# Kernel tuning notes

Hardware: AMD Instinct MI355X
Metric: run time of the kernel (lower is better)

## Reference

```python
import jax, jax.numpy as jnp
import numpy as np

N = 50000
E = 800000
IN_DIM = 128
HID = 32
HEADS = 8
OUT_DIM = 64
BN_EPS = 1e-5
NEG_SLOPE = 0.2


def batch_norm(x, gamma, beta, mean, var):
    # eval-mode BatchNorm1d using running statistics
    return (x - mean) * jax.lax.rsqrt(var + BN_EPS) * gamma + beta


def gat_conv(x, src, dst, W, att_src, att_dst, heads, out_ch, n):
    """PyG GATConv (shared src/dst lin), self-loops already included in src/dst.
    x: [n, in]; W: [in, heads*out_ch]; att_*: [heads, out_ch].
    Returns [n, heads, out_ch]."""
    h = (x @ W).reshape(n, heads, out_ch)                       # node features per head
    a_s = jnp.einsum('nho,ho->nh', h, att_src)                  # [n, heads]
    a_d = jnp.einsum('nho,ho->nh', h, att_dst)
    e = jax.nn.leaky_relu(a_s[src] + a_d[dst], NEG_SLOPE)       # [e, heads]
    # segment softmax over incoming edges of each dst node
    mx = jax.ops.segment_max(e, dst, num_segments=n)
    ex = jnp.exp(e - mx[dst])
    denom = jax.ops.segment_sum(ex, dst, num_segments=n)
    alpha = ex / (denom[dst] + 1e-16)                           # [e, heads]
    out = jax.ops.segment_sum(alpha[:, :, None] * h[src], dst, num_segments=n)
    return out                                                  # [n, heads, out_ch]


def setup_inputs() -> dict:
    key = jax.random.key(0)
    ks = jax.random.split(key, 24)
    inp = {}
    inp['x'] = jax.random.normal(ks[0], (N, IN_DIM), dtype=jnp.float32)
    inp['edge_index'] = jax.random.randint(ks[1], (2, E), 0, N, dtype=jnp.int64)
    s = 0.05
    inp['W1'] = jax.random.normal(ks[2], (IN_DIM, HEADS * HID), dtype=jnp.float32) * s
    inp['a_src1'] = jax.random.normal(ks[3], (HEADS, HID), dtype=jnp.float32) * s
    inp['a_dst1'] = jax.random.normal(ks[4], (HEADS, HID), dtype=jnp.float32) * s
    inp['b1'] = jnp.zeros((HEADS * HID,), dtype=jnp.float32)
    inp['W2'] = jax.random.normal(ks[5], (HEADS * HID, OUT_DIM), dtype=jnp.float32) * s
    inp['a_src2'] = jax.random.normal(ks[6], (1, OUT_DIM), dtype=jnp.float32) * s
    inp['a_dst2'] = jax.random.normal(ks[7], (1, OUT_DIM), dtype=jnp.float32) * s
    inp['b2'] = jnp.zeros((OUT_DIM,), dtype=jnp.float32)
    # projection Linear(out_dim -> in_dim)
    inp['Wp'] = jax.random.normal(ks[8], (OUT_DIM, IN_DIM), dtype=jnp.float32) * s
    inp['bp'] = jnp.zeros((IN_DIM,), dtype=jnp.float32)
    # BatchNorm params (eval mode running stats)
    for i, d in [(1, HEADS * HID), (2, OUT_DIM), (3, IN_DIM)]:
        k0, k1, k2, k3 = jax.random.split(ks[8 + i], 4)
        inp[f'g{i}'] = 1.0 + 0.1 * jax.random.normal(k0, (d,), dtype=jnp.float32)
        inp[f'be{i}'] = 0.1 * jax.random.normal(k1, (d,), dtype=jnp.float32)
        inp[f'm{i}'] = 0.1 * jax.random.normal(k2, (d,), dtype=jnp.float32)
        inp[f'v{i}'] = jax.random.uniform(k3, (d,), dtype=jnp.float32, minval=0.5, maxval=1.5)
    return inp


def reference(x, edge_index, W1, a_src1, a_dst1, b1, W2, a_src2, a_dst2, b2,
              Wp, bp, g1, be1, m1, v1, g2, be2, m2, v2, g3, be3, m3, v3):
    n = x.shape[0]
    loops = jnp.arange(n, dtype=edge_index.dtype)
    src = jnp.concatenate([edge_index[0], loops])   # add_self_loops=True (PyG default)
    dst = jnp.concatenate([edge_index[1], loops])

    h = gat_conv(x, src, dst, W1, a_src1, a_dst1, HEADS, HID, n)
    h = h.reshape(n, HEADS * HID) + b1              # concat=True
    h = jax.nn.elu(batch_norm(h, g1, be1, m1, v1))  # dropout is no-op in eval

    h = gat_conv(h, src, dst, W2, a_src2, a_dst2, 1, OUT_DIM, n)
    h = h.reshape(n, OUT_DIM) + b2                  # concat=False, heads=1 -> mean == identity
    h = jax.nn.elu(batch_norm(h, g2, be2, m2, v2))

    h = h @ Wp + bp
    return batch_norm(h, g3, be3, m3, v3)
```

## Files before the change

kernel.cpp:

```cpp
#include <hip/hip_runtime.h>
#include <math.h>

#define NEG_SLOPE 0.2f
#define BN_EPS 1e-5f

typedef __bf16 bf16x8 __attribute__((ext_vector_type(8)));
typedef float  f32x4  __attribute__((ext_vector_type(4)));

__device__ __forceinline__ float elu_f(float x){ return x > 0.f ? x : expm1f(x); }
__device__ __forceinline__ float lrelu_f(float x){ return x > 0.f ? x : NEG_SLOPE * x; }

__device__ __forceinline__ float b2f(ushort u){
    union { uint i; float f; } v; v.i = (uint)u << 16; return v.f;
}
__device__ __forceinline__ ushort f2b(float f){
    union { float f; uint i; } v; v.f = f;
    uint r = v.i + 0x7FFFu + ((v.i >> 16) & 1u);
    return (ushort)(r >> 16);
}

__device__ __forceinline__ bool detect_f64(const void* ei, int E, long long N)
{
    const long long* p = (const long long*)ei;
    int lane = threadIdx.x & 63;
    long long v = p[lane % max(1, min(2 * E, 64))];
    bool bad = (v < 0 || v >= N);
    return __ballot(bad) == 0ull;
}

__device__ __forceinline__ void get_edge(const void* ei, int e, int E, bool f64, int& s, int& d)
{
    if (e < E) {
        if (f64) { const long long* p = (const long long*)ei; s = (int)p[e]; d = (int)p[E + e]; }
        else     { const int*       p = (const int*)ei;       s = p[e];      d = p[E + e]; }
    } else {
        s = d = e - E;
    }
}

__global__ void setup_kernel(const void* ei, int E, int N, int* deg, int cx,
    const float* __restrict__ x, ushort* __restrict__ xb,
    const float* __restrict__ W1, const float* __restrict__ W2, const float* __restrict__ Wp,
    ushort* __restrict__ wt1, ushort* __restrict__ wt2, ushort* __restrict__ wtp,
    const float* b1, const float* b2, const float* bp,
    const float* g1, const float* be1, const float* m1, const float* v1,
    const float* g2, const float* be2, const float* m2, const float* v2,
    const float* g3, const float* be3, const float* m3, const float* v3,
    float* par)
{
    int b = blockIdx.x, t = threadIdx.x;
    if (b == 0) {
        { float s = g1[t] * rsqrtf(v1[t] + BN_EPS); par[t] = s;        par[256 + t] = b1[t] * s + be1[t] - m1[t] * s; }
        if (t < 64)  { float s = g2[t] * rsqrtf(v2[t] + BN_EPS); par[512 + t] = s;  par[576 + t] = b2[t] * s + be2[t] - m2[t] * s; }
        if (t < 128) { float s = g3[t] * rsqrtf(v3[t] + BN_EPS); par[640 + t] = s;  par[768 + t] = bp[t] * s + be3[t] - m3[t] * s; }
    } else if (b <= 224) {
        int idx = (b - 1) * 256 + t;
        if (idx < 32768) {
            int n = idx >> 7, k = idx & 127;
            wt1[idx] = f2b(W1[k * 256 + n]);
        } else if (idx < 49152) {
            int j = idx - 32768;
            int n = j >> 8, k = j & 255;
            wt2[j] = f2b(W2[k * 64 + n]);
        } else if (idx < 57344) {
            int j = idx - 49152;
            int n = j >> 6, k = j & 63;
            wtp[j] = f2b(Wp[k * 128 + n]);
        }
    } else if (b < 225 + cx) {
        long long n128 = (long long)N * 128;
        long long idx = ((long long)(b - 225) * 256 + t) * 8;
        if (idx + 7 < n128) {
            float4 v0 = *reinterpret_cast<const float4*>(&x[idx]);
            float4 v1 = *reinterpret_cast<const float4*>(&x[idx + 4]);
            ushort o[8] = { f2b(v0.x), f2b(v0.y), f2b(v0.z), f2b(v0.w),
                            f2b(v1.x), f2b(v1.y), f2b(v1.z), f2b(v1.w) };
            uint4 pk;
            pk.x = (uint)o[0] | ((uint)o[1] << 16);
            pk.y = (uint)o[2] | ((uint)o[3] << 16);
            pk.z = (uint)o[4] | ((uint)o[5] << 16);
            pk.w = (uint)o[6] | ((uint)o[7] << 16);
            *reinterpret_cast<uint4*>(&xb[idx]) = pk;
        } else {
            for (long long q = idx; q < n128; ++q) xb[q] = f2b(x[q]);
        }
    } else {
        bool f64 = detect_f64(ei, E, (long long)N);
        int i = (b - 225 - cx) * 256 + t;
        int ET = E + N;
        if (i < ET) {
            int s, d;
            get_edge(ei, i, E, f64, s, d);
            atomicAdd(&deg[d], 1);
        }
    }
}

__global__ void scan1_kernel(const int* __restrict__ deg, int N, int* __restrict__ bsum)
{
    int b = blockIdx.x, t = threadIdx.x;
    int base = b * 4096 + t * 16;
    int s = 0;
    #pragma unroll
    for (int k = 0; k < 16; k += 4) {
        int idx = base + k;
        if (idx + 3 < N) {
            int4 v = *reinterpret_cast<const int4*>(&deg[idx]);
            s += v.x + v.y + v.z + v.w;
        } else {
            for (int q = 0; q < 4; ++q) if (idx + q < N) s += deg[idx + q];
        }
    }
    #pragma unroll
    for (int off = 1; off < 64; off <<= 1) s += __shfl_xor(s, off);
    __shared__ int wsum[4];
    if ((t & 63) == 0) wsum[t >> 6] = s;
    __syncthreads();
    if (t == 0) bsum[b] = wsum[0] + wsum[1] + wsum[2] + wsum[3];
}

__global__ void scan2_kernel(const int* __restrict__ bsum, int nb, int* __restrict__ bpre)
{
    if (threadIdx.x == 0) {
        int r = 0;
        for (int i = 0; i < nb; ++i) { bpre[i] = r; r += bsum[i]; }
        bpre[nb] = r;
    }
}

__global__ void scan3_kernel(const int* __restrict__ deg, int N,
                             const int* __restrict__ bpre, int nb,
                             int* __restrict__ rowptr, int* __restrict__ fillptr)
{
    int b = blockIdx.x, t = threadIdx.x;
    int base = b * 4096 + t * 16;
    int loc[16];
    int s = 0;
    #pragma unroll
    for (int k = 0; k < 16; ++k) {
        int idx = base + k;
        int d = (idx < N) ? deg[idx] : 0;
        loc[k] = s; s += d;
    }
    int lane = t & 63;
    int incl = s;
    #pragma unroll
    for (int off = 1; off < 64; off <<= 1) {
        int v = __shfl_up(incl, off);
        if (lane >= off) incl += v;
    }
    __shared__ int wsum[4];
    if (lane == 63) wsum[t >> 6] = incl;
    __syncthreads();
    int woff = 0;
    int w = t >> 6;
    for (int i = 0; i < w; ++i) woff += wsum[i];
    int off0 = bpre[b] + woff + incl - s;
    #pragma unroll
    for (int k = 0; k < 16; ++k) {
        int idx = base + k;
        if (idx < N) { rowptr[idx] = off0 + loc[k]; fillptr[idx] = off0 + loc[k]; }
    }
    if (b == 0 && t == 0) rowptr[N] = bpre[nb];
}

__global__ void fill_kernel(const void* ei, int E, int N, int* fillptr, int* esrc)
{
    bool f64 = detect_f64(ei, E, (long long)N);
    int i = blockIdx.x * blockDim.x + threadIdx.x;
    int ET = E + N;
    if (i >= ET) return;
    int s, d;
    get_edge(ei, i, E, f64, s, d);
    int pos = atomicAdd(&fillptr[d], 1);
    esrc[pos] = s;
}

template<int ATYPE, int OMODE, int ATT>
__global__ __launch_bounds__(256) void mgemm_kernel(const void* __restrict__ Ap,
    const ushort* __restrict__ Bt, void* __restrict__ Cp, int M, int K, int NC,
    const float* __restrict__ S, const float* __restrict__ Cc,
    const float* __restrict__ att_s, const float* __restrict__ att_d,
    float* __restrict__ as_out, float* __restrict__ ad_out)
{
    const int BM = 128, LDA = 72;
    __shared__ __align__(16) ushort As[BM][LDA];
    __shared__ __align__(16) ushort Bs[64][LDA];
    __shared__ float red[128][2];
    int t = threadIdx.x;
    int m0 = blockIdx.x * BM, n0 = blockIdx.y * 64;
    int w = t >> 6, l = t & 63;
    int wm = w >> 1, wn = w & 1;
    int r16 = l & 15, kg = l >> 4;

    f32x4 acc[4][2];
    #pragma unroll
    for (int mi = 0; mi < 4; ++mi)
        #pragma unroll
        for (int ni = 0; ni < 2; ++ni)
            acc[mi][ni] = (f32x4){0.f, 0.f, 0.f, 0.f};

    for (int kb = 0; kb < K; kb += 64) {
        if (ATYPE == 0) {
            const float* A = (const float*)Ap;
            #pragma unroll
            for (int p = 0; p < 8; ++p) {
                int r = (t >> 4) + p * 16, c4 = (t & 15) * 4;
                int gm = m0 + r;
                float4 v = (gm < M) ? *reinterpret_cast<const float4*>(&A[(size_t)gm * K + kb + c4])
                                    : make_float4(0.f, 0.f, 0.f, 0.f);
                ushort4 u; u.x = f2b(v.x); u.y = f2b(v.y); u.z = f2b(v.z); u.w = f2b(v.w);
                *reinterpret_cast<ushort4*>(&As[r][c4]) = u;
            }
        } else {
            const ushort* A = (const ushort*)Ap;
            #pragma unroll
            for (int p = 0; p < 4; ++p) {
                int r = (t >> 3) + p * 32, c8 = (t & 7) * 8;
                int gm = m0 + r;
                uint4 v = (gm < M) ? *reinterpret_cast<const uint4*>(&A[(size_t)gm * K + kb + c8])
                                   : make_uint4(0u, 0u, 0u, 0u);
                *reinterpret_cast<uint4*>(&As[r][c8]) = v;
            }
        }
        #pragma unroll
        for (int p = 0; p < 2; ++p) {
            int r = (t >> 3) + p * 32, c8 = (t & 7) * 8;
            uint4 v = *reinterpret_cast<const uint4*>(&Bt[(size_t)(n0 + r) * K + kb + c8]);
            *reinterpret_cast<uint4*>(&Bs[r][c8]) = v;
        }
        __syncthreads();
        #pragma unroll
        for (int kk = 0; kk < 2; ++kk) {
            bf16x8 bB[2], bA[4];
            #pragma unroll
            for (int ni = 0; ni < 2; ++ni)
                bB[ni] = *reinterpret_cast<const bf16x8*>(&Bs[wn * 32 + ni * 16 + r16][kk * 32 + kg * 8]);
            #pragma unroll
            for (int mi = 0; mi < 4; ++mi)
                bA[mi] = *reinterpret_cast<const bf16x8*>(&As[wm * 64 + mi * 16 + r16][kk * 32 + kg * 8]);
            #pragma unroll
            for (int mi = 0; mi < 4; ++mi)
                #pragma unroll
                for (int ni = 0; ni < 2; ++ni)
                    acc[mi][ni] = __builtin_amdgcn_mfma_f32_16x16x32_bf16(bA[mi], bB[ni], acc[mi][ni], 0, 0, 0);
        }
        __syncthreads();
    }
    #pragma unroll
    for (int mi = 0; mi < 4; ++mi) {
        #pragma unroll
        for (int ni = 0; ni < 2; ++ni) {
            #pragma unroll
            for (int rg = 0; rg < 4; ++rg) {
                int gm = m0 + wm * 64 + mi * 16 + kg * 4 + rg;
                int gc = n0 + wn * 32 + ni * 16 + r16;
                if (gm < M) {
                    float v = acc[mi][ni][rg];
                    if (OMODE == 0) {
                        size_t idx = (ATT >= 1)
                            ? ((size_t)(gc >> 5) * M + gm) * 32 + (gc & 31)
                            : (size_t)gm * NC + gc;
                        ((ushort*)Cp)[idx] = f2b(v);
                    } else {
                        ((float*)Cp)[(size_t)gm * NC + gc] = v * S[gc] + Cc[gc];
                    }
                }
            }
        }
    }
    if (ATT) {
        float cs0 = att_s[n0 + wn * 32 + r16], cs1 = att_s[n0 + wn * 32 + 16 + r16];
        float cd0 = att_d[n0 + wn * 32 + r16], cd1 = att_d[n0 + wn * 32 + 16 + r16];
        float sp[4][4], dp[4][4];
        #pragma unroll
        for (int mi = 0; mi < 4; ++mi)
            #pragma unroll
            for (int rg = 0; rg < 4; ++rg) {
                sp[mi][rg] = acc[mi][0][rg] * cs0 + acc[mi][1][rg] * cs1;
                dp[mi][rg] = acc[mi][0][rg] * cd0 + acc[mi][1][rg] * cd1;
            }
        #pragma unroll
        for (int off = 1; off < 16; off <<= 1)
            #pragma unroll
            for (int mi = 0; mi < 4; ++mi)
                #pragma unroll
                for (int rg = 0; rg < 4; ++rg) {
                    sp[mi][rg] += __shfl_xor(sp[mi][rg], off);
                    dp[mi][rg] += __shfl_xor(dp[mi][rg], off);
                }
        if (ATT == 1) {
            int head = (n0 >> 5) + wn;
            if (r16 == 0) {
                #pragma unroll
                for (int mi = 0; mi < 4; ++mi)
                    #pragma unroll
                    for (int rg = 0; rg < 4; ++rg) {
                        int gm = m0 + wm * 64 + mi * 16 + kg * 4 + rg;
                        if (gm < M) {
                            as_out[(size_t)head * M + gm] = sp[mi][rg];
                            ad_out[(size_t)head * M + gm] = dp[mi][rg];
                        }
                    }
            }
        } else {
            if (wn == 1 && r16 == 0) {
                #pragma unroll
                for (int mi = 0; mi < 4; ++mi)
                    #pragma unroll
                    for (int rg = 0; rg < 4; ++rg) {
                        int r = wm * 64 + mi * 16 + kg * 4 + rg;
                        red[r][0] = sp[mi][rg];
                        red[r][1] = dp[mi][rg];
                    }
            }
            __syncthreads();
            if (wn == 0 && r16 == 0) {
                #pragma unroll
                for (int mi = 0; mi < 4; ++mi)
                    #pragma unroll
                    for (int rg = 0; rg < 4; ++rg) {
                        int r = wm * 64 + mi * 16 + kg * 4 + rg;
                        int gm = m0 + r;
                        if (gm < M) {
                            as_out[gm] = sp[mi][rg] + red[r][0];
                            ad_out[gm] = dp[mi][rg] + red[r][1];
                        }
                    }
            }
        }
    }
}

template<int NS, bool SATT>
__global__ void agg_kernel(const ushort* __restrict__ hs,
                           const float* __restrict__ ast, const float* __restrict__ adt,
                           const int* __restrict__ rowptr, const int* __restrict__ esrc,
                           const float* __restrict__ Sv, const float* __restrict__ Cv,
                           ushort* __restrict__ outb, int N)
{
    int s = blockIdx.x & (NS - 1);
    int wslot = threadIdx.x >> 6;
    int lane = threadIdx.x & 63;
    int qq = lane >> 4;
    int row = wslot * 4 + qq;
    int n = (int)(blockIdx.x / NS) * 16 + row;
    bool active = (n < N);
    int beg = 0, end = 0;
    float adv = 0.f;
    if (active) {
        beg = rowptr[n];
        end = rowptr[n + 1];
        adv = SATT ? adt[(size_t)s * N + n] : adt[n];
    }
    const float* as_s = SATT ? (ast + (size_t)s * N) : ast;
    const char* slabc = (const char*)(hs + (size_t)s * N * 32);
    int sub = (lane >> 3) & 1;
    uint eoff = (uint)(lane & 7) * 8u;
    float den = 0.f;
    float acc[4] = {0.f, 0.f, 0.f, 0.f};

    auto body = [&](float av, uint2 r) {
        float w = __expf(lrelu_f(av + adv));
        den += w;
        union { uint u; float f; } c;
        c.u = r.x << 16;         acc[0] += w * c.f;
        c.u = r.x & 0xffff0000u; acc[1] += w * c.f;
        c.u = r.y << 16;         acc[2] += w * c.f;
        c.u = r.y & 0xffff0000u; acc[3] += w * c.f;
    };

    int e = beg + sub;
    for (; e + 6 < end; e += 8) {
        int s0 = esrc[e], s1 = esrc[e + 2], s2 = esrc[e + 4], s3 = esrc[e + 6];
        float a0 = as_s[s0], a1 = as_s[s1], a2 = as_s[s2], a3 = as_s[s3];
        uint2 r0 = *reinterpret_cast<const uint2*>(slabc + ((uint)s0 * 64u + eoff));
        uint2 r1 = *reinterpret_cast<const uint2*>(slabc + ((uint)s1 * 64u + eoff));
        uint2 r2 = *reinterpret_cast<const uint2*>(slabc + ((uint)s2 * 64u + eoff));
        uint2 r3 = *reinterpret_cast<const uint2*>(slabc + ((uint)s3 * 64u + eoff));
        body(a0, r0); body(a1, r1); body(a2, r2); body(a3, r3);
    }
    for (; e < end; e += 2) {
        int s0 = esrc[e];
        float a0 = as_s[s0];
        uint2 r0 = *reinterpret_cast<const uint2*>(slabc + ((uint)s0 * 64u + eoff));
        body(a0, r0);
    }

    den += __shfl_xor(den, 1, 64);
    den += __shfl_xor(den, 2, 64);
    den += __shfl_xor(den, 4, 64);
    den += __shfl_xor(den, 8, 64);
    #pragma unroll
    for (int f = 0; f < 4; ++f) acc[f] += __shfl_xor(acc[f], 8, 64);
    if (active && sub == 0) {
        float inv = 8.f / (den + 8e-16f);
        int f = s * 32 + (lane & 7) * 4;
        float4 Sc = *reinterpret_cast<const float4*>(&Sv[f]);
        float4 Cc = *reinterpret_cast<const float4*>(&Cv[f]);
        ushort4 o;
        o.x = f2b(elu_f(acc[0] * inv * Sc.x + Cc.x));
        o.y = f2b(elu_f(acc[1] * inv * Sc.y + Cc.y));
        o.z = f2b(elu_f(acc[2] * inv * Sc.z + Cc.z));
        o.w = f2b(elu_f(acc[3] * inv * Sc.w + Cc.w));
        *reinterpret_cast<ushort4*>(&outb[(size_t)n * (NS * 32) + f]) = o;
    }
}

extern "C" void kernel_launch(void* const* d_in, const int* in_sizes, int n_in,
                              void* d_out, int out_size, void* d_ws, size_t ws_size,
                              hipStream_t stream)
{
    const float* x      = (const float*)d_in[0];
    const void*  ei     = d_in[1];
    const float* W1     = (const float*)d_in[2];
    const float* a_src1 = (const float*)d_in[3];
    const float* a_dst1 = (const float*)d_in[4];
    const float* b1     = (const float*)d_in[5];
    const float* W2     = (const float*)d_in[6];
    const float* a_src2 = (const float*)d_in[7];
    const float* a_dst2 = (const float*)d_in[8];
    const float* b2     = (const float*)d_in[9];
    const float* Wp     = (const float*)d_in[10];
    const float* bp     = (const float*)d_in[11];
    const float* g1 = (const float*)d_in[12], *be1 = (const float*)d_in[13];
    const float* m1 = (const float*)d_in[14], *v1  = (const float*)d_in[15];
    const float* g2 = (const float*)d_in[16], *be2 = (const float*)d_in[17];
    const float* m2 = (const float*)d_in[18], *v2  = (const float*)d_in[19];
    const float* g3 = (const float*)d_in[20], *be3 = (const float*)d_in[21];
    const float* m3 = (const float*)d_in[22], *v3  = (const float*)d_in[23];
    float* out = (float*)d_out;

    const int N  = in_sizes[0] / 128;
    const int E  = in_sizes[1] / 2;
    const int ET = E + N;

    char* base = (char*)d_ws;
    size_t off = 0;
    auto alloc = [&](size_t bytes) -> char* {
        char* p = base + off;
        off += (bytes + 255) & ~(size_t)255;
        return p;
    };
    float*  par     = (float*)alloc(1024 * 4);
    int*    bsum    = (int*)alloc(256);
    int*    bpre    = (int*)alloc(256);
    int*    rowptr  = (int*)alloc((size_t)(N + 1) * 4);
    int*    fillptr = (int*)alloc((size_t)(N + 1) * 4);
    int*    esrc    = (int*)alloc((size_t)ET * 4);
    float*  as1     = (float*)alloc((size_t)N * 8 * 4);
    float*  ad1     = (float*)alloc((size_t)N * 8 * 4);
    float*  as2     = (float*)alloc((size_t)N * 4);
    float*  ad2     = (float*)alloc((size_t)N * 4);
    ushort* wt1     = (ushort*)alloc(256 * 128 * 2);
    ushort* wt2     = (ushort*)alloc(64 * 256 * 2);
    ushort* wtp     = (ushort*)alloc(128 * 64 * 2);
    ushort* xb      = (ushort*)alloc((size_t)N * 128 * 2);
    ushort* h1      = (ushort*)alloc((size_t)N * 256 * 2);
    ushort* h1b     = (ushort*)alloc((size_t)N * 256 * 2);
    ushort* h2      = (ushort*)alloc((size_t)N * 64 * 2);
    ushort* g2buf   = (ushort*)alloc((size_t)N * 64 * 2);

    hipMemsetAsync(fillptr, 0, (N + 1) * sizeof(int), stream);
    int cx = (int)(((size_t)N * 128 + 2047) / 2048);
    int cblocks = (ET + 255) / 256;
    setup_kernel<<<225 + cx + cblocks, 256, 0, stream>>>(ei, E, N, fillptr, cx,
        x, xb, W1, W2, Wp, wt1, wt2, wtp,
        b1, b2, bp, g1, be1, m1, v1, g2, be2, m2, v2, g3, be3, m3, v3, par);

    int nb = (N + 4095) / 4096;
    scan1_kernel<<<nb, 256, 0, stream>>>(fillptr, N, bsum);
    scan2_kernel<<<1, 64, 0, stream>>>(bsum, nb, bpre);
    scan3_kernel<<<nb, 256, 0, stream>>>(fillptr, N, bpre, nb, rowptr, fillptr);
    fill_kernel<<<cblocks, 256, 0, stream>>>(ei, E, N, fillptr, esrc);

    int mb128 = (N + 127) / 128;
    int ngrp16 = (N + 15) / 16;
    mgemm_kernel<1, 0, 1><<<dim3(mb128, 4), 256, 0, stream>>>(xb, wt1, h1, N, 128, 256,
        nullptr, nullptr, a_src1, a_dst1, as1, ad1);
    agg_kernel<8, true><<<ngrp16 * 8, 256, 0, stream>>>(h1, as1, ad1, rowptr, esrc,
        par, par + 256, h1b, N);

    mgemm_kernel<1, 0, 2><<<dim3(mb128, 1), 256, 0, stream>>>(h1b, wt2, h2, N, 256, 64,
        nullptr, nullptr, a_src2, a_dst2, as2, ad2);
    agg_kernel<2, false><<<ngrp16 * 2, 256, 0, stream>>>(h2, as2, ad2, rowptr, esrc,
        par + 512, par + 576, g2buf, N);

    mgemm_kernel<1, 1, 0><<<dim3(mb128, 2), 256, 0, stream>>>(g2buf, wtp, out, N, 64, 128,
        par + 640, par + 768, nullptr, nullptr, nullptr, nullptr);
}
```

Before: 280.6 us.

## Replace layer-1 attention aggregation with MFMA-based block sparse matmul kernel

Layer-1 aggregation becomes a new spmm1 kernel. Each block handles 16 destination nodes and processes their incoming edges in chunks of 32. The kernel computes unnormalised exp attention weights into a bf16 block-diagonal A tile in LDS, gathers source feature rows into LDS, and accumulates with bf16 MFMA, then normalises by the per-row denominators and applies the BN+ELU epilogue. The layer-1 GEMM now writes h1 row-major and attention scores node-major to suit the new gather pattern. The max subtraction is dropped from the softmax, and the exp weights are rounded to bf16. This risks overflow or small accuracy changes, and the MFMA tiles are mostly zeros because each edge belongs to only one row.

```diff
diff --git a/kernel.cpp b/kernel.cpp
--- a/kernel.cpp
+++ b/kernel.cpp
@@ -258,7 +258,7 @@
                 if (gm < M) {
                     float v = acc[mi][ni][rg];
                     if (OMODE == 0) {
-                        size_t idx = (ATT >= 1)
+                        size_t idx = (ATT == 2)
                             ? ((size_t)(gc >> 5) * M + gm) * 32 + (gc & 31)
                             : (size_t)gm * NC + gc;
                         ((ushort*)Cp)[idx] = f2b(v);
@@ -298,8 +298,8 @@
                     for (int rg = 0; rg < 4; ++rg) {
                         int gm = m0 + wm * 64 + mi * 16 + kg * 4 + rg;
                         if (gm < M) {
-                            as_out[(size_t)head * M + gm] = sp[mi][rg];
-                            ad_out[(size_t)head * M + gm] = dp[mi][rg];
+                            as_out[(size_t)gm * 8 + head] = sp[mi][rg];
+                            ad_out[(size_t)gm * 8 + head] = dp[mi][rg];
                         }
                     }
             }
@@ -327,6 +327,106 @@
                             ad_out[gm] = dp[mi][rg] + red[r][1];
                         }
                     }
+            }
+        }
+    }
+}
+
+__global__ __launch_bounds__(256) void spmm1_kernel(
+    const ushort* __restrict__ h1,
+    const float* __restrict__ as1,
+    const float* __restrict__ ad1,
+    const int* __restrict__ rowptr,
+    const int* __restrict__ esrc,
+    const float* __restrict__ par,
+    ushort* __restrict__ outb, int N)
+{
+    __shared__ ushort B_lds[32][264];
+    __shared__ ushort A_lds[8][16][48];
+    __shared__ float  den_lds[16][8];
+    __shared__ int    rowp[17];
+    __shared__ int    src_lds[32];
+    int t = threadIdx.x;
+    int g = blockIdx.x;
+    int n0 = g * 16;
+
+    if (t < 17) rowp[t] = rowptr[min(n0 + t, N)];
+    if (t < 128) ((float*)den_lds)[t] = 0.f;
+    {
+        ushort* A0 = &A_lds[0][0][0];
+        uint4 z = make_uint4(0u, 0u, 0u, 0u);
+        *reinterpret_cast<uint4*>(A0 + t * 24 + 0)  = z;
+        *reinterpret_cast<uint4*>(A0 + t * 24 + 8)  = z;
+        *reinterpret_cast<uint4*>(A0 + t * 24 + 16) = z;
+    }
+    __syncthreads();
+
+    int e0 = rowp[0], e1 = rowp[16];
+    int lane = t & 63;
+    int wv = t >> 6;
+    int r16 = lane & 15, kg = lane >> 4;
+    int slot = t >> 3, hh = t & 7;
+
+    f32x4 acc[4];
+    #pragma unroll
+    for (int i = 0; i < 4; ++i) acc[i] = (f32x4){0.f, 0.f, 0.f, 0.f};
+
+    int pz_row = -1;
+
+    for (int cb = e0; cb < e1; cb += 32) {
+        int cnt = min(32, e1 - cb);
+        if (pz_row >= 0) A_lds[hh][pz_row][slot] = 0;
+        pz_row = -1;
+        {
+            int sl_src = 0;
+            if (slot < cnt) {
+                int ge = cb + slot;
+                sl_src = esrc[ge];
+                int r = 0;
+                while (r < 15 && ge >= rowp[r + 1]) ++r;
+                float wval = __expf(lrelu_f(as1[(size_t)sl_src * 8 + hh] +
+                                            ad1[(size_t)(n0 + r) * 8 + hh]));
+                A_lds[hh][r][slot] = f2b(wval);
+                atomicAdd(&den_lds[r][hh], wval);
+                pz_row = r;
+            }
+            if (hh == 0) src_lds[slot] = sl_src;
+        }
+        __syncthreads();
+        #pragma unroll
+        for (int rr = 0; rr < 4; ++rr) {
+            int idx = t + rr * 256;
+            int e = idx >> 5, c = idx & 31;
+            uint4 v = *reinterpret_cast<const uint4*>(&h1[(size_t)src_lds[e] * 256 + c * 8]);
+            *reinterpret_cast<uint4*>(&B_lds[e][c * 8]) = v;
+        }
+        __syncthreads();
+        bf16x8 a0 = *reinterpret_cast<const bf16x8*>(&A_lds[2 * wv][r16][kg * 8]);
+        bf16x8 a1 = *reinterpret_cast<const bf16x8*>(&A_lds[2 * wv + 1][r16][kg * 8]);
+        #pragma unroll
+        for (int tt = 0; tt < 4; ++tt) {
+            int col = wv * 64 + tt * 16 + r16;
+            union { bf16x8 v; ushort u[8]; } bb;
+            #pragma unroll
+            for (int j = 0; j < 8; ++j) bb.u[j] = B_lds[kg * 8 + j][col];
+            acc[tt] = __builtin_amdgcn_mfma_f32_16x16x32_bf16((tt < 2) ? a0 : a1, bb.v, acc[tt], 0, 0, 0);
+        }
+        __syncthreads();
+    }
+
+    #pragma unroll
+    for (int tt = 0; tt < 4; ++tt) {
+        int head = 2 * wv + (tt >> 1);
+        int col = wv * 64 + tt * 16 + r16;
+        float Sv = par[col], Cv = par[256 + col];
+        #pragma unroll
+        for (int rg = 0; rg < 4; ++rg) {
+            int row = kg * 4 + rg;
+            int n = n0 + row;
+            if (n < N) {
+                float inv = 1.f / (den_lds[row][head] + 1e-16f);
+                float v = elu_f(acc[tt][rg] * inv * Sv + Cv);
+                outb[(size_t)n * 256 + col] = f2b(v);
             }
         }
     }
@@ -478,8 +578,7 @@
     int ngrp16 = (N + 15) / 16;
     mgemm_kernel<1, 0, 1><<<dim3(mb128, 4), 256, 0, stream>>>(xb, wt1, h1, N, 128, 256,
         nullptr, nullptr, a_src1, a_dst1, as1, ad1);
-    agg_kernel<8, true><<<ngrp16 * 8, 256, 0, stream>>>(h1, as1, ad1, rowptr, esrc,
-        par, par + 256, h1b, N);
+    spmm1_kernel<<<ngrp16, 256, 0, stream>>>(h1, as1, ad1, rowptr, esrc, par, h1b, N);
 
     mgemm_kernel<1, 0, 2><<<dim3(mb128, 1), 256, 0, stream>>>(h1b, wt2, h2, N, 256, 64,
         nullptr, nullptr, a_src2, a_dst2, as2, ad2);
```

Result: slower. 302.9 us (+7.9%).
